# Kernel optimization log

Hardware: AMD Instinct MI355X
Metric: run time of the kernel (lower is better)

## Reference

```python
import jax, jax.numpy as jnp
import numpy as np

N_NODES = 100000


def setup_inputs() -> dict:
    key = jax.random.key(0)
    k1, k2, k3, k4, k5, k6 = jax.random.split(key, 6)
    n, e, d_in, d_out = N_NODES, 1600000, 256, 256
    features = jax.random.normal(k1, (n, d_in), dtype=jnp.float32)
    edge_src = jax.random.randint(k2, (e,), 0, n, dtype=jnp.int32)
    edge_dst = jax.random.randint(k3, (e,), 0, n, dtype=jnp.int32)
    edge_weight = jax.random.uniform(k4, (e,), dtype=jnp.float32)
    a = 1.0 / np.sqrt(d_out)
    W = jax.random.uniform(k5, (d_out, d_in), dtype=jnp.float32, minval=-a, maxval=a)
    b = jax.random.uniform(k6, (d_out,), dtype=jnp.float32, minval=-a, maxval=a)
    return {"features": features, "edge_src": edge_src, "edge_dst": edge_dst,
            "edge_weight": edge_weight, "W": W, "b": b}


def reference(features, edge_src, edge_dst, edge_weight, W, b):
    # SpMM: out[i] = sum_{(j->i) in E} a_ij * features[j]
    msgs = features[edge_src] * edge_weight[:, None]          # [E, d_in]
    agg = jax.ops.segment_sum(msgs, edge_dst, num_segments=N_NODES)  # [n, d_in]
    # Dense projection (nn.Linear: x @ W.T + b)
    return agg @ W.T + b
```

## Files before the change

kernel.cpp:

```cpp
#include <hip/hip_runtime.h>
#include <hip/hip_bf16.h>

#define D 256
#define SCAN_CHUNK 2048

typedef __attribute__((ext_vector_type(8))) short bf16x8;
typedef __attribute__((ext_vector_type(4))) float f32x4;
typedef __attribute__((ext_vector_type(4))) unsigned short u16x4;
typedef __attribute__((ext_vector_type(8))) unsigned short u16x8;

__global__ void __launch_bounds__(256) hist_kernel(
    const int* __restrict__ dst, int* __restrict__ counts, int E) {
  int i = blockIdx.x * 256 + threadIdx.x;
  if (i < E) atomicAdd(&counts[dst[i]], 1);
}

__global__ void __launch_bounds__(256) scan_chunk_sum(
    const int* __restrict__ counts, int* __restrict__ chunk_sum, int N) {
  __shared__ int lds[256];
  const int t = threadIdx.x;
  const int base = blockIdx.x * SCAN_CHUNK + t * 8;
  int s = 0;
#pragma unroll
  for (int j = 0; j < 8; ++j) {
    int i = base + j;
    if (i < N) s += counts[i];
  }
  lds[t] = s;
  __syncthreads();
  for (int off = 128; off > 0; off >>= 1) {
    if (t < off) lds[t] += lds[t + off];
    __syncthreads();
  }
  if (t == 0) chunk_sum[blockIdx.x] = lds[0];
}

__global__ void __launch_bounds__(64) scan_chunk_off(
    const int* __restrict__ chunk_sum, int* __restrict__ chunk_off, int NC,
    int* __restrict__ offsets, int N, int E) {
  if (threadIdx.x == 0) {
    int run = 0;
    for (int c = 0; c < NC; ++c) {
      chunk_off[c] = run;
      run += chunk_sum[c];
    }
    offsets[N] = E;
  }
}

__global__ void __launch_bounds__(256) scan_finalize(
    int* __restrict__ counts_cursor, int* __restrict__ offsets,
    const int* __restrict__ chunk_off, int N) {
  __shared__ int lds[256];
  const int t = threadIdx.x;
  const int base_i = blockIdx.x * SCAN_CHUNK + t * 8;
  int c[8];
  int s = 0;
#pragma unroll
  for (int j = 0; j < 8; ++j) {
    int i = base_i + j;
    c[j] = (i < N) ? counts_cursor[i] : 0;
    s += c[j];
  }
  lds[t] = s;
  __syncthreads();
  for (int off = 1; off < 256; off <<= 1) {
    int v = (t >= off) ? lds[t - off] : 0;
    __syncthreads();
    lds[t] += v;
    __syncthreads();
  }
  int run = chunk_off[blockIdx.x] + ((t > 0) ? lds[t - 1] : 0);
#pragma unroll
  for (int j = 0; j < 8; ++j) {
    int i = base_i + j;
    if (i < N) {
      offsets[i] = run;
      counts_cursor[i] = run;
      run += c[j];
    }
  }
}

__global__ void __launch_bounds__(256) fill_kernel(
    const int* __restrict__ dst, int* __restrict__ cursor,
    int* __restrict__ csr_eid, int E) {
  int i = blockIdx.x * 256 + threadIdx.x;
  if (i >= E) return;
  int pos = atomicAdd(&cursor[dst[i]], 1);
  csr_eid[pos] = i;
}

__device__ __forceinline__ unsigned short f2b_u(float f) {
  __hip_bfloat16 h = __float2bfloat16(f);
  return *reinterpret_cast<unsigned short*>(&h);
}

__global__ void __launch_bounds__(256) cvt_feat_kernel(
    const float* __restrict__ feat, unsigned short* __restrict__ fb,
    long long n) {
  long long i = ((long long)blockIdx.x * 256 + threadIdx.x) * 8;
  if (i >= n) return;
  f32x4 a = *(const f32x4*)(feat + i);
  f32x4 b = *(const f32x4*)(feat + i + 4);
  u16x8 r;
  r[0] = f2b_u(a[0]); r[1] = f2b_u(a[1]); r[2] = f2b_u(a[2]); r[3] = f2b_u(a[3]);
  r[4] = f2b_u(b[0]); r[5] = f2b_u(b[1]); r[6] = f2b_u(b[2]); r[7] = f2b_u(b[3]);
  *(u16x8*)(fb + i) = r;
}

__device__ __forceinline__ float b2f(unsigned short u) {
  unsigned int x = ((unsigned int)u) << 16;
  return __builtin_bit_cast(float, x);
}

__global__ void __launch_bounds__(256) gather_bf16_kernel(
    const unsigned short* __restrict__ fb, const int* __restrict__ offsets,
    const int* __restrict__ csr_eid, const int* __restrict__ src,
    const float* __restrict__ ew, float* __restrict__ out, int N) {
  int node = (blockIdx.x * 256 + threadIdx.x) >> 6;
  int lane = threadIdx.x & 63;
  if (node >= N) return;
  int e = offsets[node];
  const int end = offsets[node + 1];
  float4 acc = {0.f, 0.f, 0.f, 0.f};
  for (; e + 2 <= end; e += 2) {
    int i0 = csr_eid[e], i1 = csr_eid[e + 1];
    int s0 = src[i0], s1 = src[i1];
    float w0 = ew[i0], w1 = ew[i1];
    u16x4 v0 = *(const u16x4*)(fb + (size_t)s0 * D + lane * 4);
    u16x4 v1 = *(const u16x4*)(fb + (size_t)s1 * D + lane * 4);
    acc.x = fmaf(b2f(v0[0]), w0, acc.x); acc.y = fmaf(b2f(v0[1]), w0, acc.y);
    acc.z = fmaf(b2f(v0[2]), w0, acc.z); acc.w = fmaf(b2f(v0[3]), w0, acc.w);
    acc.x = fmaf(b2f(v1[0]), w1, acc.x); acc.y = fmaf(b2f(v1[1]), w1, acc.y);
    acc.z = fmaf(b2f(v1[2]), w1, acc.z); acc.w = fmaf(b2f(v1[3]), w1, acc.w);
  }
  if (e < end) {
    int i0 = csr_eid[e];
    int s0 = src[i0];
    float w0 = ew[i0];
    u16x4 v0 = *(const u16x4*)(fb + (size_t)s0 * D + lane * 4);
    acc.x = fmaf(b2f(v0[0]), w0, acc.x); acc.y = fmaf(b2f(v0[1]), w0, acc.y);
    acc.z = fmaf(b2f(v0[2]), w0, acc.z); acc.w = fmaf(b2f(v0[3]), w0, acc.w);
  }
  *(float4*)(out + (size_t)node * D + lane * 4) = acc;
}

__global__ void __launch_bounds__(256) gather_kernel(
    const float* __restrict__ feat, const int* __restrict__ offsets,
    const int* __restrict__ csr_eid, const int* __restrict__ src,
    const float* __restrict__ ew, float* __restrict__ out, int N) {
  int node = (blockIdx.x * 256 + threadIdx.x) >> 6;
  int lane = threadIdx.x & 63;
  if (node >= N) return;
  int e = offsets[node];
  const int end = offsets[node + 1];
  float4 acc = {0.f, 0.f, 0.f, 0.f};
  for (; e + 2 <= end; e += 2) {
    int i0 = csr_eid[e], i1 = csr_eid[e + 1];
    int s0 = src[i0], s1 = src[i1];
    float w0 = ew[i0], w1 = ew[i1];
    float4 v0 = *(const float4*)(feat + (size_t)s0 * D + lane * 4);
    float4 v1 = *(const float4*)(feat + (size_t)s1 * D + lane * 4);
    acc.x = fmaf(v0.x, w0, acc.x); acc.y = fmaf(v0.y, w0, acc.y);
    acc.z = fmaf(v0.z, w0, acc.z); acc.w = fmaf(v0.w, w0, acc.w);
    acc.x = fmaf(v1.x, w1, acc.x); acc.y = fmaf(v1.y, w1, acc.y);
    acc.z = fmaf(v1.z, w1, acc.z); acc.w = fmaf(v1.w, w1, acc.w);
  }
  if (e < end) {
    int i0 = csr_eid[e];
    int s0 = src[i0];
    float w0 = ew[i0];
    float4 v0 = *(const float4*)(feat + (size_t)s0 * D + lane * 4);
    acc.x = fmaf(v0.x, w0, acc.x); acc.y = fmaf(v0.y, w0, acc.y);
    acc.z = fmaf(v0.z, w0, acc.z); acc.w = fmaf(v0.w, w0, acc.w);
  }
  *(float4*)(out + (size_t)node * D + lane * 4) = acc;
}

__global__ void __launch_bounds__(256) scatter_edges(
    const float* __restrict__ feat, const int* __restrict__ src,
    const int* __restrict__ dst, const float* __restrict__ ew,
    float* __restrict__ agg, int E) {
  int gid = blockIdx.x * 256 + threadIdx.x;
  int e = gid >> 6;
  int lane = threadIdx.x & 63;
  if (e >= E) return;
  int s = src[e];
  int d = dst[e];
  float wt = ew[e];
  const float4 v = *(const float4*)(feat + (size_t)s * D + lane * 4);
  float* o = agg + (size_t)d * D + lane * 4;
  unsafeAtomicAdd(o + 0, v.x * wt);
  unsafeAtomicAdd(o + 1, v.y * wt);
  unsafeAtomicAdd(o + 2, v.z * wt);
  unsafeAtomicAdd(o + 3, v.w * wt);
}

__device__ __forceinline__ short f2b(float f) {
  __hip_bfloat16 h = __float2bfloat16(f);
  return *reinterpret_cast<short*>(&h);
}

__device__ __forceinline__ bf16x8 load_cvt8(const float* p) {
  f32x4 a = *(const f32x4*)p;
  f32x4 b = *(const f32x4*)(p + 4);
  bf16x8 r;
  r[0] = f2b(a[0]); r[1] = f2b(a[1]); r[2] = f2b(a[2]); r[3] = f2b(a[3]);
  r[4] = f2b(b[0]); r[5] = f2b(b[1]); r[6] = f2b(b[2]); r[7] = f2b(b[3]);
  return r;
}

__global__ void __launch_bounds__(256) proj_mfma(
    float* __restrict__ io, const float* __restrict__ W,
    const float* __restrict__ bias, int M) {
  const int tid = threadIdx.x;
  const int wave = tid >> 6;
  const int lane = tid & 63;
  const int lrow = lane & 15;
  const int lkg = lane >> 4;

  const int m0 = blockIdx.x * 64;
  const int n0 = wave * 64;

  f32x4 acc[4][4] = {};

  const float* arow0;
  const float* arow1;
  const float* arow2;
  const float* arow3;
  {
    int r0 = min(m0 + 0 * 16 + lrow, M - 1);
    int r1 = min(m0 + 1 * 16 + lrow, M - 1);
    int r2 = min(m0 + 2 * 16 + lrow, M - 1);
    int r3 = min(m0 + 3 * 16 + lrow, M - 1);
    arow0 = io + (size_t)r0 * D + lkg * 8;
    arow1 = io + (size_t)r1 * D + lkg * 8;
    arow2 = io + (size_t)r2 * D + lkg * 8;
    arow3 = io + (size_t)r3 * D + lkg * 8;
  }
  const float* brow0 = W + (size_t)(n0 + 0 * 16 + lrow) * D + lkg * 8;
  const float* brow1 = W + (size_t)(n0 + 1 * 16 + lrow) * D + lkg * 8;
  const float* brow2 = W + (size_t)(n0 + 2 * 16 + lrow) * D + lkg * 8;
  const float* brow3 = W + (size_t)(n0 + 3 * 16 + lrow) * D + lkg * 8;

#pragma unroll
  for (int kk = 0; kk < 8; ++kk) {
    bf16x8 af[4], bf[4];
    af[0] = load_cvt8(arow0 + kk * 32);
    af[1] = load_cvt8(arow1 + kk * 32);
    af[2] = load_cvt8(arow2 + kk * 32);
    af[3] = load_cvt8(arow3 + kk * 32);
    bf[0] = load_cvt8(brow0 + kk * 32);
    bf[1] = load_cvt8(brow1 + kk * 32);
    bf[2] = load_cvt8(brow2 + kk * 32);
    bf[3] = load_cvt8(brow3 + kk * 32);
#pragma unroll
    for (int mb = 0; mb < 4; ++mb)
#pragma unroll
      for (int nb = 0; nb < 4; ++nb)
        acc[mb][nb] = __builtin_amdgcn_mfma_f32_16x16x32_bf16(
            af[mb], bf[nb], acc[mb][nb], 0, 0, 0);
  }

  __syncthreads();

  float bv[4];
#pragma unroll
  for (int nb = 0; nb < 4; ++nb) bv[nb] = bias[n0 + nb * 16 + lrow];

#pragma unroll
  for (int mb = 0; mb < 4; ++mb) {
#pragma unroll
    for (int reg = 0; reg < 4; ++reg) {
      int r = m0 + mb * 16 + lkg * 4 + reg;
      if (r < M) {
#pragma unroll
        for (int nb = 0; nb < 4; ++nb)
          io[(size_t)r * D + n0 + nb * 16 + lrow] = acc[mb][nb][reg] + bv[nb];
      }
    }
  }
}

extern "C" void kernel_launch(void* const* d_in, const int* in_sizes, int n_in,
                              void* d_out, int out_size, void* d_ws, size_t ws_size,
                              hipStream_t stream) {
  const float* feat = (const float*)d_in[0];
  const int* src = (const int*)d_in[1];
  const int* dst = (const int*)d_in[2];
  const float* ew = (const float*)d_in[3];
  const float* W = (const float*)d_in[4];
  const float* bias = (const float*)d_in[5];
  float* out = (float*)d_out;

  const int E = in_sizes[1];
  const int M = out_size / D;
  const long long nfeat = in_sizes[0];
  const int NC = (M + SCAN_CHUNK - 1) / SCAN_CHUNK;

  size_t off_b = ((size_t)(M + 1) * 4 + 255) & ~(size_t)255;
  size_t cur_b = ((size_t)M * 4 + 255) & ~(size_t)255;
  size_t eid_b = ((size_t)E * 4 + 255) & ~(size_t)255;
  size_t chk_b = ((size_t)(2 * NC) * 4 + 255) & ~(size_t)255;
  size_t fb_b = ((size_t)nfeat * 2 + 255) & ~(size_t)255;
  size_t need_csr = off_b + cur_b + eid_b + chk_b;
  size_t need_bf16 = need_csr + fb_b;

  if (ws_size >= need_csr && d_ws != nullptr) {
    char* ws = (char*)d_ws;
    int* offsets = (int*)ws;
    int* cursor = (int*)(ws + off_b);
    int* csr_eid = (int*)(ws + off_b + cur_b);
    int* chunk_sum = (int*)(ws + off_b + cur_b + eid_b);
    int* chunk_off = chunk_sum + NC;
    unsigned short* fb = (unsigned short*)(ws + need_csr);

    const int eb = (E + 255) / 256;
    const bool use_bf16 = (ws_size >= need_bf16);

    if (use_bf16) {
      int cb = (int)((nfeat / 8 + 255) / 256);
      cvt_feat_kernel<<<cb, 256, 0, stream>>>(feat, fb, nfeat);
    }

    hipMemsetAsync(cursor, 0, (size_t)M * 4, stream);
    hist_kernel<<<eb, 256, 0, stream>>>(dst, cursor, E);
    scan_chunk_sum<<<NC, 256, 0, stream>>>(cursor, chunk_sum, M);
    scan_chunk_off<<<1, 64, 0, stream>>>(chunk_sum, chunk_off, NC, offsets, M, E);
    scan_finalize<<<NC, 256, 0, stream>>>(cursor, offsets, chunk_off, M);
    fill_kernel<<<eb, 256, 0, stream>>>(dst, cursor, csr_eid, E);

    long long threads = (long long)M * 64;
    int blocks = (int)((threads + 255) / 256);
    if (use_bf16) {
      gather_bf16_kernel<<<blocks, 256, 0, stream>>>(fb, offsets, csr_eid, src,
                                                     ew, out, M);
    } else {
      gather_kernel<<<blocks, 256, 0, stream>>>(feat, offsets, csr_eid, src,
                                                ew, out, M);
    }
  } else {
    hipMemsetAsync(out, 0, (size_t)out_size * sizeof(float), stream);
    long long threads = (long long)E * 64;
    int blocks = (int)((threads + 255) / 256);
    scatter_edges<<<blocks, 256, 0, stream>>>(feat, src, dst, ew, out, E);
  }

  proj_mfma<<<(M + 63) / 64, 256, 0, stream>>>(out, W, bias, M);
}
```

Baseline: 691.3 us.

## Project features before aggregation and gather packed src/weight pairs

Reorders the computation so the dense projection is applied to the node features first (Y = X·Wᵀ stored as bf16), and the sparse aggregation then runs over the projected rows with bias added in the gather epilogue. This removes the separate feature conversion pass and the in-place projection of the aggregate. The CSR fill now writes packed (src, weight) pairs, so the gather avoids the extra csr_eid→src/ew indirection, and each node uses 32 lanes with 16-byte loads. Rounding the projected values to bf16 before summation changes the numerical error profile, and the pair array costs more workspace.

```diff
diff --git a/kernel.cpp b/kernel.cpp
--- a/kernel.cpp
+++ b/kernel.cpp
@@ -82,6 +82,16 @@
   }
 }
 
+__global__ void __launch_bounds__(256) fill_pair_kernel(
+    const int* __restrict__ src, const int* __restrict__ dst,
+    const float* __restrict__ ew, int* __restrict__ cursor,
+    int2* __restrict__ pairs, int E) {
+  int i = blockIdx.x * 256 + threadIdx.x;
+  if (i >= E) return;
+  int pos = atomicAdd(&cursor[dst[i]], 1);
+  pairs[pos] = make_int2(src[i], __float_as_int(ew[i]));
+}
+
 __global__ void __launch_bounds__(256) fill_kernel(
     const int* __restrict__ dst, int* __restrict__ cursor,
     int* __restrict__ csr_eid, int E) {
@@ -94,6 +104,138 @@
 __device__ __forceinline__ unsigned short f2b_u(float f) {
   __hip_bfloat16 h = __float2bfloat16(f);
   return *reinterpret_cast<unsigned short*>(&h);
+}
+__device__ __forceinline__ short f2b(float f) {
+  __hip_bfloat16 h = __float2bfloat16(f);
+  return *reinterpret_cast<short*>(&h);
+}
+__device__ __forceinline__ float b2f(unsigned short u) {
+  unsigned int x = ((unsigned int)u) << 16;
+  return __builtin_bit_cast(float, x);
+}
+__device__ __forceinline__ bf16x8 load_cvt8(const float* p) {
+  f32x4 a = *(const f32x4*)p;
+  f32x4 b = *(const f32x4*)(p + 4);
+  bf16x8 r;
+  r[0] = f2b(a[0]); r[1] = f2b(a[1]); r[2] = f2b(a[2]); r[3] = f2b(a[3]);
+  r[4] = f2b(b[0]); r[5] = f2b(b[1]); r[6] = f2b(b[2]); r[7] = f2b(b[3]);
+  return r;
+}
+
+__global__ void __launch_bounds__(256) proj_feat_mfma(
+    const float* __restrict__ feat, const float* __restrict__ W,
+    unsigned short* __restrict__ Y, int M) {
+  const int tid = threadIdx.x;
+  const int wave = tid >> 6;
+  const int lane = tid & 63;
+  const int lrow = lane & 15;
+  const int lkg = lane >> 4;
+
+  const int m0 = blockIdx.x * 64;
+  const int n0 = wave * 64;
+
+  f32x4 acc[4][4] = {};
+
+  const float* arow0;
+  const float* arow1;
+  const float* arow2;
+  const float* arow3;
+  {
+    int r0 = min(m0 + 0 * 16 + lrow, M - 1);
+    int r1 = min(m0 + 1 * 16 + lrow, M - 1);
+    int r2 = min(m0 + 2 * 16 + lrow, M - 1);
+    int r3 = min(m0 + 3 * 16 + lrow, M - 1);
+    arow0 = feat + (size_t)r0 * D + lkg * 8;
+    arow1 = feat + (size_t)r1 * D + lkg * 8;
+    arow2 = feat + (size_t)r2 * D + lkg * 8;
+    arow3 = feat + (size_t)r3 * D + lkg * 8;
+  }
+  const float* brow0 = W + (size_t)(n0 + 0 * 16 + lrow) * D + lkg * 8;
+  const float* brow1 = W + (size_t)(n0 + 1 * 16 + lrow) * D + lkg * 8;
+  const float* brow2 = W + (size_t)(n0 + 2 * 16 + lrow) * D + lkg * 8;
+  const float* brow3 = W + (size_t)(n0 + 3 * 16 + lrow) * D + lkg * 8;
+
+#pragma unroll
+  for (int kk = 0; kk < 8; ++kk) {
+    bf16x8 af[4], bf[4];
+    af[0] = load_cvt8(arow0 + kk * 32);
+    af[1] = load_cvt8(arow1 + kk * 32);
+    af[2] = load_cvt8(arow2 + kk * 32);
+    af[3] = load_cvt8(arow3 + kk * 32);
+    bf[0] = load_cvt8(brow0 + kk * 32);
+    bf[1] = load_cvt8(brow1 + kk * 32);
+    bf[2] = load_cvt8(brow2 + kk * 32);
+    bf[3] = load_cvt8(brow3 + kk * 32);
+#pragma unroll
+    for (int mb = 0; mb < 4; ++mb)
+#pragma unroll
+      for (int nb = 0; nb < 4; ++nb)
+        acc[mb][nb] = __builtin_amdgcn_mfma_f32_16x16x32_bf16(
+            af[mb], bf[nb], acc[mb][nb], 0, 0, 0);
+  }
+
+#pragma unroll
+  for (int mb = 0; mb < 4; ++mb) {
+#pragma unroll
+    for (int reg = 0; reg < 4; ++reg) {
+      int r = m0 + mb * 16 + lkg * 4 + reg;
+      if (r < M) {
+#pragma unroll
+        for (int nb = 0; nb < 4; ++nb)
+          Y[(size_t)r * D + n0 + nb * 16 + lrow] = f2b_u(acc[mb][nb][reg]);
+      }
+    }
+  }
+}
+
+__global__ void __launch_bounds__(256) gather_pair_kernel(
+    const unsigned short* __restrict__ Y, const int* __restrict__ offsets,
+    const int2* __restrict__ pairs, const float* __restrict__ bias,
+    float* __restrict__ out, int N) {
+  int node = (blockIdx.x * 256 + threadIdx.x) >> 5;
+  int sub = threadIdx.x & 31;
+  if (node >= N) return;
+  int e = offsets[node];
+  const int end = offsets[node + 1];
+  float acc[8] = {0.f, 0.f, 0.f, 0.f, 0.f, 0.f, 0.f, 0.f};
+  const int d0 = sub * 8;
+
+  for (; e + 4 <= end; e += 4) {
+    int2 p0 = pairs[e + 0];
+    int2 p1 = pairs[e + 1];
+    int2 p2 = pairs[e + 2];
+    int2 p3 = pairs[e + 3];
+    u16x8 v0 = *(const u16x8*)(Y + (size_t)p0.x * D + d0);
+    u16x8 v1 = *(const u16x8*)(Y + (size_t)p1.x * D + d0);
+    u16x8 v2 = *(const u16x8*)(Y + (size_t)p2.x * D + d0);
+    u16x8 v3 = *(const u16x8*)(Y + (size_t)p3.x * D + d0);
+    float w0 = __int_as_float(p0.y);
+    float w1 = __int_as_float(p1.y);
+    float w2 = __int_as_float(p2.y);
+    float w3 = __int_as_float(p3.y);
+#pragma unroll
+    for (int j = 0; j < 8; ++j) {
+      acc[j] = fmaf(b2f(v0[j]), w0, acc[j]);
+      acc[j] = fmaf(b2f(v1[j]), w1, acc[j]);
+      acc[j] = fmaf(b2f(v2[j]), w2, acc[j]);
+      acc[j] = fmaf(b2f(v3[j]), w3, acc[j]);
+    }
+  }
+  for (; e < end; ++e) {
+    int2 p0 = pairs[e];
+    u16x8 v0 = *(const u16x8*)(Y + (size_t)p0.x * D + d0);
+    float w0 = __int_as_float(p0.y);
+#pragma unroll
+    for (int j = 0; j < 8; ++j) acc[j] = fmaf(b2f(v0[j]), w0, acc[j]);
+  }
+
+  f32x4 bv0 = *(const f32x4*)(bias + d0);
+  f32x4 bv1 = *(const f32x4*)(bias + d0 + 4);
+  float* o = out + (size_t)node * D + d0;
+  f32x4 r0 = {acc[0] + bv0[0], acc[1] + bv0[1], acc[2] + bv0[2], acc[3] + bv0[3]};
+  f32x4 r1 = {acc[4] + bv1[0], acc[5] + bv1[1], acc[6] + bv1[2], acc[7] + bv1[3]};
+  *(f32x4*)o = r0;
+  *(f32x4*)(o + 4) = r1;
 }
 
 __global__ void __launch_bounds__(256) cvt_feat_kernel(
@@ -107,11 +249,6 @@
   r[0] = f2b_u(a[0]); r[1] = f2b_u(a[1]); r[2] = f2b_u(a[2]); r[3] = f2b_u(a[3]);
   r[4] = f2b_u(b[0]); r[5] = f2b_u(b[1]); r[6] = f2b_u(b[2]); r[7] = f2b_u(b[3]);
   *(u16x8*)(fb + i) = r;
-}
-
-__device__ __forceinline__ float b2f(unsigned short u) {
-  unsigned int x = ((unsigned int)u) << 16;
-  return __builtin_bit_cast(float, x);
 }
 
 __global__ void __launch_bounds__(256) gather_bf16_kernel(
@@ -197,20 +334,6 @@
   unsafeAtomicAdd(o + 3, v.w * wt);
 }
 
-__device__ __forceinline__ short f2b(float f) {
-  __hip_bfloat16 h = __float2bfloat16(f);
-  return *reinterpret_cast<short*>(&h);
-}
-
-__device__ __forceinline__ bf16x8 load_cvt8(const float* p) {
-  f32x4 a = *(const f32x4*)p;
-  f32x4 b = *(const f32x4*)(p + 4);
-  bf16x8 r;
-  r[0] = f2b(a[0]); r[1] = f2b(a[1]); r[2] = f2b(a[2]); r[3] = f2b(a[3]);
-  r[4] = f2b(b[0]); r[5] = f2b(b[1]); r[6] = f2b(b[2]); r[7] = f2b(b[3]);
-  return r;
-}
-
 __global__ void __launch_bounds__(256) proj_mfma(
     float* __restrict__ io, const float* __restrict__ W,
     const float* __restrict__ bias, int M) {
@@ -301,29 +424,56 @@
 
   size_t off_b = ((size_t)(M + 1) * 4 + 255) & ~(size_t)255;
   size_t cur_b = ((size_t)M * 4 + 255) & ~(size_t)255;
+  size_t chk_b = ((size_t)(2 * NC) * 4 + 255) & ~(size_t)255;
   size_t eid_b = ((size_t)E * 4 + 255) & ~(size_t)255;
-  size_t chk_b = ((size_t)(2 * NC) * 4 + 255) & ~(size_t)255;
-  size_t fb_b = ((size_t)nfeat * 2 + 255) & ~(size_t)255;
-  size_t need_csr = off_b + cur_b + eid_b + chk_b;
-  size_t need_bf16 = need_csr + fb_b;
-
-  if (ws_size >= need_csr && d_ws != nullptr) {
+  size_t pair_b = ((size_t)E * 8 + 255) & ~(size_t)255;
+  size_t y_b = ((size_t)nfeat * 2 + 255) & ~(size_t)255;
+
+  size_t need_A = off_b + cur_b + chk_b + pair_b + y_b;
+  size_t need_B = off_b + cur_b + chk_b + eid_b + y_b;
+  size_t need_C = off_b + cur_b + chk_b + eid_b;
+
+  const int eb = (E + 255) / 256;
+
+  if (ws_size >= need_A && d_ws != nullptr) {
     char* ws = (char*)d_ws;
     int* offsets = (int*)ws;
     int* cursor = (int*)(ws + off_b);
-    int* csr_eid = (int*)(ws + off_b + cur_b);
-    int* chunk_sum = (int*)(ws + off_b + cur_b + eid_b);
+    int* chunk_sum = (int*)(ws + off_b + cur_b);
     int* chunk_off = chunk_sum + NC;
-    unsigned short* fb = (unsigned short*)(ws + need_csr);
-
-    const int eb = (E + 255) / 256;
-    const bool use_bf16 = (ws_size >= need_bf16);
+    int2* pairs = (int2*)(ws + off_b + cur_b + chk_b);
+    unsigned short* Y = (unsigned short*)(ws + off_b + cur_b + chk_b + pair_b);
+
+    proj_feat_mfma<<<(M + 63) / 64, 256, 0, stream>>>(feat, W, Y, M);
+
+    hipMemsetAsync(cursor, 0, (size_t)M * 4, stream);
+    hist_kernel<<<eb, 256, 0, stream>>>(dst, cursor, E);
+    scan_chunk_sum<<<NC, 256, 0, stream>>>(cursor, chunk_sum, M);
+    scan_chunk_off<<<1, 64, 0, stream>>>(chunk_sum, chunk_off, NC, offsets, M, E);
+    scan_finalize<<<NC, 256, 0, stream>>>(cursor, offsets, chunk_off, M);
+    fill_pair_kernel<<<eb, 256, 0, stream>>>(src, dst, ew, cursor, pairs, E);
+
+    long long threads = (long long)M * 32;
+    int blocks = (int)((threads + 255) / 256);
+    gather_pair_kernel<<<blocks, 256, 0, stream>>>(Y, offsets, pairs, bias,
+                                                   out, M);
+    return;
+  }
+
+  if (ws_size >= need_C && d_ws != nullptr) {
+    char* ws = (char*)d_ws;
+    int* offsets = (int*)ws;
+    int* cursor = (int*)(ws + off_b);
+    int* chunk_sum = (int*)(ws + off_b + cur_b);
+    int* chunk_off = chunk_sum + NC;
+    int* csr_eid = (int*)(ws + off_b + cur_b + chk_b);
+    unsigned short* fb = (unsigned short*)(ws + off_b + cur_b + chk_b + eid_b);
+    const bool use_bf16 = (ws_size >= need_B);
 
     if (use_bf16) {
       int cb = (int)((nfeat / 8 + 255) / 256);
       cvt_feat_kernel<<<cb, 256, 0, stream>>>(feat, fb, nfeat);
     }
-
     hipMemsetAsync(cursor, 0, (size_t)M * 4, stream);
     hist_kernel<<<eb, 256, 0, stream>>>(dst, cursor, E);
     scan_chunk_sum<<<NC, 256, 0, stream>>>(cursor, chunk_sum, M);
```

Result: faster. 573.5 us (-17.1%).
